# Kernel tuning notes

Measured on AMD Instinct MI355X. Metric: run time of the kernel, lower is better.

Reference implementation:

```python
import jax, jax.numpy as jnp
import numpy as np

DIM = 512
HEADS = 8
DIM_HEAD = 64
INNER = HEADS * DIM_HEAD
MAX_POS = 512


def setup_inputs() -> dict:
    key = jax.random.key(0)
    ks = jax.random.split(key, 6)
    b, n = 8, 1024
    x = jax.random.normal(ks[0], (b, n, DIM), dtype=jnp.float32)
    Wq = jax.random.normal(ks[1], (DIM, INNER), dtype=jnp.float32) * (DIM ** -0.5)
    Wkv = jax.random.normal(ks[2], (DIM, 2 * INNER), dtype=jnp.float32) * (DIM ** -0.5)
    rel_emb = jax.random.normal(ks[3], (2 * MAX_POS + 1, DIM_HEAD), dtype=jnp.float32) * 0.02
    Wo = jax.random.normal(ks[4], (INNER, DIM), dtype=jnp.float32) * (INNER ** -0.5)
    bo = jnp.zeros((DIM,), dtype=jnp.float32)
    return {"x": x, "Wq": Wq, "Wkv": Wkv, "rel_emb": rel_emb, "Wo": Wo, "bo": bo}


def reference(x, Wq, Wkv, rel_emb, Wo, bo):
    b, n, _ = x.shape
    scale = DIM_HEAD ** -0.5
    q = x @ Wq                      # [b, n, inner]
    kv = x @ Wkv                    # [b, n, 2*inner]
    k, v = jnp.split(kv, 2, axis=-1)
    # b n (h d) -> b h n d
    split_heads = lambda t: t.reshape(b, n, HEADS, DIM_HEAD).transpose(0, 2, 1, 3)
    q, k, v = split_heads(q), split_heads(k), split_heads(v)
    dots = jnp.einsum('bhid,bhjd->bhij', q, k) * scale  # [b,h,n,n]
    seq = jnp.arange(n)
    dist = jnp.clip(seq[:, None] - seq[None, :], -MAX_POS, MAX_POS) + MAX_POS  # [n,n]
    rel = rel_emb[dist]                                  # [n, n, d]
    pos_attn = jnp.einsum('bhnd,nrd->bhnr', q, rel) * scale
    dots = dots + pos_attn
    attn = jax.nn.softmax(dots, axis=-1)
    out = jnp.einsum('bhij,bhjd->bhid', attn, v)        # [b,h,n,d]
    out = out.transpose(0, 2, 1, 3).reshape(b, n, INNER)
    return out @ Wo + bo
```

## Files before the change

kernel.cpp:

```cpp
#include <hip/hip_runtime.h>

typedef __attribute__((ext_vector_type(8))) short bf16x8;
typedef __attribute__((ext_vector_type(4))) float f32x4;
typedef unsigned short u16;
typedef unsigned int u32;

#define MFMA16(a, b, c) __builtin_amdgcn_mfma_f32_16x16x32_bf16((a), (b), (c), 0, 0, 0)

__device__ __forceinline__ u16 f2b(float f) {
    u32 u = __float_as_uint(f);
    u32 r = u + 0x7fffu + ((u >> 16) & 1u);
    return (u16)(r >> 16);
}
__device__ __forceinline__ float b2f(u16 u) { return __uint_as_float(((u32)u) << 16); }

__global__ void k_f32_to_bf16(const float* __restrict__ in, u16* __restrict__ out, int n) {
    int i = (blockIdx.x * blockDim.x + threadIdx.x) * 4;
    if (i + 3 < n) {
        float4 v = *(const float4*)(in + i);
        out[i] = f2b(v.x); out[i + 1] = f2b(v.y); out[i + 2] = f2b(v.z); out[i + 3] = f2b(v.w);
    } else {
        for (int j = i; j < n; ++j) out[j] = f2b(in[j]);
    }
}

__global__ void k_make_wqkv_t(const float* __restrict__ Wq, const float* __restrict__ Wkv,
                              u16* __restrict__ wt) {
    int tid = blockIdx.x * blockDim.x + threadIdx.x;
    int k = tid & 511, n = tid >> 9;
    float v = (n < 512) ? Wq[k * 512 + n] : Wkv[k * 1024 + (n - 512)];
    wt[n * 512 + k] = f2b(v);
}

__global__ void k_make_wo_t(const float* __restrict__ Wo, u16* __restrict__ wt) {
    int tid = blockIdx.x * blockDim.x + threadIdx.x;
    int k = tid & 511, n = tid >> 9;
    wt[n * 512 + k] = f2b(Wo[k * 512 + n]);
}

__global__ __launch_bounds__(256) void k_gemm_qkv(const u16* __restrict__ A, const u16* __restrict__ Bt,
                                                  u16* __restrict__ Q, u16* __restrict__ K,
                                                  u16* __restrict__ V) {
    __shared__ u16 As[128][40];
    __shared__ u16 Bs[128][40];
    const int t = threadIdx.x, l = t & 63, w = t >> 6;
    const int wr = w >> 1, wc = w & 1, l15 = l & 15, lg = l >> 4;
    const int m0 = blockIdx.x * 128, n0 = blockIdx.y * 128;
    f32x4 acc[4][4];
#pragma unroll
    for (int i = 0; i < 4; ++i)
#pragma unroll
        for (int j = 0; j < 4; ++j) acc[i][j] = (f32x4){0.f, 0.f, 0.f, 0.f};
    const int sr = t >> 1, sko = (t & 1) * 16;
    for (int k0 = 0; k0 < 512; k0 += 32) {
        __syncthreads();
        {
            const bf16x8* pa = (const bf16x8*)(A + (size_t)(m0 + sr) * 512 + k0 + sko);
            *(bf16x8*)&As[sr][sko] = pa[0];
            *(bf16x8*)&As[sr][sko + 8] = pa[1];
            const bf16x8* pb = (const bf16x8*)(Bt + (size_t)(n0 + sr) * 512 + k0 + sko);
            *(bf16x8*)&Bs[sr][sko] = pb[0];
            *(bf16x8*)&Bs[sr][sko + 8] = pb[1];
        }
        __syncthreads();
        bf16x8 af[4], bfr[4];
#pragma unroll
        for (int rt = 0; rt < 4; ++rt) af[rt] = *(const bf16x8*)&As[wr * 64 + rt * 16 + l15][lg * 8];
#pragma unroll
        for (int ct = 0; ct < 4; ++ct) bfr[ct] = *(const bf16x8*)&Bs[wc * 64 + ct * 16 + l15][lg * 8];
#pragma unroll
        for (int rt = 0; rt < 4; ++rt)
#pragma unroll
            for (int ct = 0; ct < 4; ++ct) acc[rt][ct] = MFMA16(af[rt], bfr[ct], acc[rt][ct]);
    }
#pragma unroll
    for (int rt = 0; rt < 4; ++rt)
#pragma unroll
        for (int ct = 0; ct < 4; ++ct) {
            int n = n0 + wc * 64 + ct * 16 + l15;
            int sec = n >> 9, nn = n & 511, h = nn >> 6, d = nn & 63;
            u16* dst = (sec == 0) ? Q : ((sec == 1) ? K : V);
#pragma unroll
            for (int r = 0; r < 4; ++r) {
                int m = m0 + wr * 64 + rt * 16 + lg * 4 + r;
                int b = m >> 10, pos = m & 1023, bh = b * 8 + h;
                dst[(size_t)bh * 65536 + (size_t)pos * 64 + d] = f2b(acc[rt][ct][r]);
            }
        }
}

__global__ __launch_bounds__(256) void k_transpose_v(const u16* __restrict__ V, u16* __restrict__ Vt) {
    __shared__ u16 tile[64][72];
    const int bh = blockIdx.x >> 4, pt = blockIdx.x & 15;
    const int p0 = pt * 64;
    const int t = threadIdx.x, r = t >> 2, c0 = (t & 3) * 16;
    const bf16x8* src = (const bf16x8*)(V + (size_t)bh * 65536 + (size_t)(p0 + r) * 64 + c0);
    *(bf16x8*)&tile[r][c0] = src[0];
    *(bf16x8*)&tile[r][c0 + 8] = src[1];
    __syncthreads();
    union { u16 u[8]; bf16x8 v; } o0, o1;
#pragma unroll
    for (int ii = 0; ii < 8; ++ii) {
        o0.u[ii] = tile[c0 + ii][r];
        o1.u[ii] = tile[c0 + 8 + ii][r];
    }
    bf16x8* dst = (bf16x8*)(Vt + (size_t)bh * 65536 + (size_t)r * 1024 + p0 + c0);
    dst[0] = o0.v;
    dst[1] = o1.v;
}

__global__ __launch_bounds__(512, 4) void k_attn(const u16* __restrict__ Q, const u16* __restrict__ K,
                                                 const u16* __restrict__ Vt, const u16* __restrict__ relb,
                                                 u16* __restrict__ Ob) {
    __shared__ u16 Ks[64][72];
    __shared__ u16 Vs[64][72];
    __shared__ u16 sdw[8][16][84];
    __shared__ u16 pw[8][16][72];
    const int t = threadIdx.x, l = t & 63, w = t >> 6;
    const int l15 = l & 15, lg = l >> 4;
    const int g = (blockIdx.x & 7) * 64 + (blockIdx.x >> 3);
    const int bh = g >> 3;
    const int iw = (g & 7) * 128 + w * 16;
    const size_t hb = (size_t)bh * 65536;
    const int srow = t >> 3, scol = (t & 7) * 8;

    bf16x8 qf[2];
#pragma unroll
    for (int kf = 0; kf < 2; ++kf)
        qf[kf] = *(const bf16x8*)(Q + hb + (size_t)(iw + l15) * 64 + kf * 32 + lg * 8);

    f32x4 acc_o[4];
    float m_r[4], l_r[4];
#pragma unroll
    for (int i = 0; i < 4; ++i) {
        acc_o[i] = (f32x4){0.f, 0.f, 0.f, 0.f};
        m_r[i] = -1e30f;
        l_r[i] = 0.f;
    }

    bf16x8 kreg = *(const bf16x8*)(K + hb + (size_t)srow * 64 + scol);
    bf16x8 vreg = *(const bf16x8*)(Vt + hb + (size_t)srow * 1024 + scol);
    *(bf16x8*)&Ks[srow][scol] = kreg;
    *(bf16x8*)&Vs[srow][scol] = vreg;
    kreg = *(const bf16x8*)(K + hb + (size_t)(64 + srow) * 64 + scol);
    vreg = *(const bf16x8*)(Vt + hb + (size_t)srow * 1024 + 64 + scol);
    __syncthreads();

    for (int j0 = 0; j0 < 1024; j0 += 64) {
        f32x4 acc_s[4];
#pragma unroll
        for (int c = 0; c < 4; ++c) {
            acc_s[c] = (f32x4){0.f, 0.f, 0.f, 0.f};
#pragma unroll
            for (int kf = 0; kf < 2; ++kf) {
                bf16x8 kb = *(const bf16x8*)&Ks[c * 16 + l15][kf * 32 + lg * 8];
                acc_s[c] = MFMA16(qf[kf], kb, acc_s[c]);
            }
        }
        const int bd = iw - j0 - 63;
#pragma unroll
        for (int pt = 0; pt < 5; ++pt) {
            int tcol = pt * 16 + l15;
            int dd = bd + tcol;
            dd = dd < -512 ? -512 : (dd > 512 ? 512 : dd);
            const u16* rrow = relb + (size_t)(dd + 512) * 64;
            f32x4 a = (f32x4){0.f, 0.f, 0.f, 0.f};
#pragma unroll
            for (int kf = 0; kf < 2; ++kf) {
                bf16x8 rb = *(const bf16x8*)(rrow + kf * 32 + lg * 8);
                a = MFMA16(qf[kf], rb, a);
            }
#pragma unroll
            for (int r = 0; r < 4; ++r) sdw[w][lg * 4 + r][tcol] = f2b(a[r]);
        }
#pragma unroll
        for (int rr = 0; rr < 4; ++rr) {
            const int row = lg * 4 + rr;
            const int tb = row + 63 - l15;
            float sv[4];
#pragma unroll
            for (int c = 0; c < 4; ++c)
                sv[c] = (acc_s[c][rr] + b2f(sdw[w][row][tb - c * 16])) * 0.125f;
            float mt = fmaxf(fmaxf(sv[0], sv[1]), fmaxf(sv[2], sv[3]));
#pragma unroll
            for (int off = 1; off < 16; off <<= 1) mt = fmaxf(mt, __shfl_xor(mt, off, 64));
            float mnew = fmaxf(m_r[rr], mt);
            float alpha = __expf(m_r[rr] - mnew);
            m_r[rr] = mnew;
            float rs = 0.f;
#pragma unroll
            for (int c = 0; c < 4; ++c) {
                float pv = __expf(sv[c] - mnew);
                rs += pv;
                pw[w][row][c * 16 + l15] = f2b(pv);
            }
#pragma unroll
            for (int off = 1; off < 16; off <<= 1) rs += __shfl_xor(rs, off, 64);
            l_r[rr] = l_r[rr] * alpha + rs;
#pragma unroll
            for (int dt = 0; dt < 4; ++dt) acc_o[dt][rr] *= alpha;
        }
        bf16x8 pa[2];
#pragma unroll
        for (int kf = 0; kf < 2; ++kf) pa[kf] = *(const bf16x8*)&pw[w][l15][kf * 32 + lg * 8];
#pragma unroll
        for (int dt = 0; dt < 4; ++dt) {
#pragma unroll
            for (int kf = 0; kf < 2; ++kf) {
                bf16x8 vb = *(const bf16x8*)&Vs[dt * 16 + l15][kf * 32 + lg * 8];
                acc_o[dt] = MFMA16(pa[kf], vb, acc_o[dt]);
            }
        }
        __syncthreads();
        if (j0 + 64 < 1024) {
            *(bf16x8*)&Ks[srow][scol] = kreg;
            *(bf16x8*)&Vs[srow][scol] = vreg;
            if (j0 + 128 < 1024) {
                kreg = *(const bf16x8*)(K + hb + (size_t)(j0 + 128 + srow) * 64 + scol);
                vreg = *(const bf16x8*)(Vt + hb + (size_t)srow * 1024 + (j0 + 128) + scol);
            }
            __syncthreads();
        }
    }
    const int b = bh >> 3, h = bh & 7;
#pragma unroll
    for (int rr = 0; rr < 4; ++rr) {
        float rinv = 1.0f / l_r[rr];
        int row = lg * 4 + rr;
#pragma unroll
        for (int dt = 0; dt < 4; ++dt)
            Ob[(size_t)(b * 1024 + iw + row) * 512 + h * 64 + dt * 16 + l15] = f2b(acc_o[dt][rr] * rinv);
    }
}

__global__ __launch_bounds__(256) void k_gemm_out(const u16* __restrict__ A, const u16* __restrict__ Bt,
                                                  const float* __restrict__ bias, float* __restrict__ out) {
    __shared__ u16 As[128][40];
    __shared__ u16 Bs[128][40];
    const int t = threadIdx.x, l = t & 63, w = t >> 6;
    const int wr = w >> 1, wc = w & 1, l15 = l & 15, lg = l >> 4;
    const int m0 = blockIdx.x * 128, n0 = blockIdx.y * 128;
    f32x4 acc[4][4];
#pragma unroll
    for (int i = 0; i < 4; ++i)
#pragma unroll
        for (int j = 0; j < 4; ++j) acc[i][j] = (f32x4){0.f, 0.f, 0.f, 0.f};
    const int sr = t >> 1, sko = (t & 1) * 16;
    for (int k0 = 0; k0 < 512; k0 += 32) {
        __syncthreads();
        {
            const bf16x8* pa = (const bf16x8*)(A + (size_t)(m0 + sr) * 512 + k0 + sko);
            *(bf16x8*)&As[sr][sko] = pa[0];
            *(bf16x8*)&As[sr][sko + 8] = pa[1];
            const bf16x8* pb = (const bf16x8*)(Bt + (size_t)(n0 + sr) * 512 + k0 + sko);
            *(bf16x8*)&Bs[sr][sko] = pb[0];
            *(bf16x8*)&Bs[sr][sko + 8] = pb[1];
        }
        __syncthreads();
        bf16x8 af[4], bfr[4];
#pragma unroll
        for (int rt = 0; rt < 4; ++rt) af[rt] = *(const bf16x8*)&As[wr * 64 + rt * 16 + l15][lg * 8];
#pragma unroll
        for (int ct = 0; ct < 4; ++ct) bfr[ct] = *(const bf16x8*)&Bs[wc * 64 + ct * 16 + l15][lg * 8];
#pragma unroll
        for (int rt = 0; rt < 4; ++rt)
#pragma unroll
            for (int ct = 0; ct < 4; ++ct) acc[rt][ct] = MFMA16(af[rt], bfr[ct], acc[rt][ct]);
    }
#pragma unroll
    for (int rt = 0; rt < 4; ++rt)
#pragma unroll
        for (int ct = 0; ct < 4; ++ct) {
            int n = n0 + wc * 64 + ct * 16 + l15;
            float bv = bias[n];
#pragma unroll
            for (int r = 0; r < 4; ++r) {
                int m = m0 + wr * 64 + rt * 16 + lg * 4 + r;
                out[(size_t)m * 512 + n] = acc[rt][ct][r] + bv;
            }
        }
}

extern "C" void kernel_launch(void* const* d_in, const int* in_sizes, int n_in,
                              void* d_out, int out_size, void* d_ws, size_t ws_size,
                              hipStream_t stream) {
    const float* x    = (const float*)d_in[0];
    const float* Wq   = (const float*)d_in[1];
    const float* Wkv  = (const float*)d_in[2];
    const float* rel  = (const float*)d_in[3];
    const float* Wo   = (const float*)d_in[4];
    const float* bo   = (const float*)d_in[5];
    float* out = (float*)d_out;
    char* ws = (char*)d_ws;

    u16* xb   = (u16*)(ws + 0);
    u16* wqkv = (u16*)(ws + 8388608);
    u16* wot  = (u16*)(ws + 9961472);
    u16* relb = (u16*)(ws + 10485760);
    u16* Q    = (u16*)(ws + 10616960);
    u16* K    = (u16*)(ws + 19005568);
    u16* V    = (u16*)(ws + 27394176);
    u16* Vt   = (u16*)(ws + 35782784);
    u16* Ob   = (u16*)(ws + 44171392);

    k_f32_to_bf16<<<4096, 256, 0, stream>>>(x, xb, 4194304);
    k_f32_to_bf16<<<65, 256, 0, stream>>>(rel, relb, 65600);
    k_make_wqkv_t<<<3072, 256, 0, stream>>>(Wq, Wkv, wqkv);
    k_make_wo_t<<<1024, 256, 0, stream>>>(Wo, wot);
    k_gemm_qkv<<<dim3(64, 12), 256, 0, stream>>>(xb, wqkv, Q, K, V);
    k_transpose_v<<<1024, 256, 0, stream>>>(V, Vt);
    k_attn<<<512, 512, 0, stream>>>(Q, K, Vt, relb, Ob);
    k_gemm_out<<<dim3(64, 4), 256, 0, stream>>>(Ob, wot, bo, out);
}
```

Baseline: 145.0 us.

## Transpose attention MFMAs so softmax rows stay in registers, drop P LDS staging

Swaps the MFMA operand order so each lane holds a full query row's scores (S^T layout). Softmax then needs only two cross-lane shuffles, and P can be packed directly into registers as the B operand of the PV MFMA, with no round trip through shared memory. The relative-position band is stored as packed u32 pairs. A __syncthreads is added after the band write, occupancy hint is lowered from 4 to 2 blocks, and V is read as two 4-element halves to match the new K-index layout.

```diff
diff --git a/kernel.cpp b/kernel.cpp
--- a/kernel.cpp
+++ b/kernel.cpp
@@ -1,6 +1,7 @@
 #include <hip/hip_runtime.h>
 
 typedef __attribute__((ext_vector_type(8))) short bf16x8;
+typedef __attribute__((ext_vector_type(4))) short bf16x4;
 typedef __attribute__((ext_vector_type(4))) float f32x4;
 typedef unsigned short u16;
 typedef unsigned int u32;
@@ -13,6 +14,9 @@
     return (u16)(r >> 16);
 }
 __device__ __forceinline__ float b2f(u16 u) { return __uint_as_float(((u32)u) << 16); }
+__device__ __forceinline__ u32 packbf(float lo, float hi) {
+    return (u32)f2b(lo) | ((u32)f2b(hi) << 16);
+}
 
 __global__ void k_f32_to_bf16(const float* __restrict__ in, u16* __restrict__ out, int n) {
     int i = (blockIdx.x * blockDim.x + threadIdx.x) * 4;
@@ -109,13 +113,12 @@
     dst[1] = o1.v;
 }
 
-__global__ __launch_bounds__(512, 4) void k_attn(const u16* __restrict__ Q, const u16* __restrict__ K,
+__global__ __launch_bounds__(512, 2) void k_attn(const u16* __restrict__ Q, const u16* __restrict__ K,
                                                  const u16* __restrict__ Vt, const u16* __restrict__ relb,
                                                  u16* __restrict__ Ob) {
     __shared__ u16 Ks[64][72];
     __shared__ u16 Vs[64][72];
-    __shared__ u16 sdw[8][16][84];
-    __shared__ u16 pw[8][16][72];
+    __shared__ u32 sdw[8][16][42];
     const int t = threadIdx.x, l = t & 63, w = t >> 6;
     const int l15 = l & 15, lg = l >> 4;
     const int g = (blockIdx.x & 7) * 64 + (blockIdx.x >> 3);
@@ -130,13 +133,9 @@
         qf[kf] = *(const bf16x8*)(Q + hb + (size_t)(iw + l15) * 64 + kf * 32 + lg * 8);
 
     f32x4 acc_o[4];
-    float m_r[4], l_r[4];
-#pragma unroll
-    for (int i = 0; i < 4; ++i) {
-        acc_o[i] = (f32x4){0.f, 0.f, 0.f, 0.f};
-        m_r[i] = -1e30f;
-        l_r[i] = 0.f;
-    }
+#pragma unroll
+    for (int i = 0; i < 4; ++i) acc_o[i] = (f32x4){0.f, 0.f, 0.f, 0.f};
+    float m_r = -1e30f, l_r = 0.f;
 
     bf16x8 kreg = *(const bf16x8*)(K + hb + (size_t)srow * 64 + scol);
     bf16x8 vreg = *(const bf16x8*)(Vt + hb + (size_t)srow * 1024 + scol);
@@ -154,83 +153,98 @@
 #pragma unroll
             for (int kf = 0; kf < 2; ++kf) {
                 bf16x8 kb = *(const bf16x8*)&Ks[c * 16 + l15][kf * 32 + lg * 8];
-                acc_s[c] = MFMA16(qf[kf], kb, acc_s[c]);
+                acc_s[c] = MFMA16(kb, qf[kf], acc_s[c]);
             }
         }
         const int bd = iw - j0 - 63;
 #pragma unroll
         for (int pt = 0; pt < 5; ++pt) {
-            int tcol = pt * 16 + l15;
-            int dd = bd + tcol;
+            int dd = bd + pt * 16 + l15;
             dd = dd < -512 ? -512 : (dd > 512 ? 512 : dd);
             const u16* rrow = relb + (size_t)(dd + 512) * 64;
             f32x4 a = (f32x4){0.f, 0.f, 0.f, 0.f};
 #pragma unroll
             for (int kf = 0; kf < 2; ++kf) {
                 bf16x8 rb = *(const bf16x8*)(rrow + kf * 32 + lg * 8);
-                a = MFMA16(qf[kf], rb, a);
-            }
-#pragma unroll
-            for (int r = 0; r < 4; ++r) sdw[w][lg * 4 + r][tcol] = f2b(a[r]);
-        }
-#pragma unroll
-        for (int rr = 0; rr < 4; ++rr) {
-            const int row = lg * 4 + rr;
-            const int tb = row + 63 - l15;
-            float sv[4];
-#pragma unroll
-            for (int c = 0; c < 4; ++c)
-                sv[c] = (acc_s[c][rr] + b2f(sdw[w][row][tb - c * 16])) * 0.125f;
-            float mt = fmaxf(fmaxf(sv[0], sv[1]), fmaxf(sv[2], sv[3]));
-#pragma unroll
-            for (int off = 1; off < 16; off <<= 1) mt = fmaxf(mt, __shfl_xor(mt, off, 64));
-            float mnew = fmaxf(m_r[rr], mt);
-            float alpha = __expf(m_r[rr] - mnew);
-            m_r[rr] = mnew;
-            float rs = 0.f;
-#pragma unroll
-            for (int c = 0; c < 4; ++c) {
-                float pv = __expf(sv[c] - mnew);
-                rs += pv;
-                pw[w][row][c * 16 + l15] = f2b(pv);
-            }
-#pragma unroll
-            for (int off = 1; off < 16; off <<= 1) rs += __shfl_xor(rs, off, 64);
-            l_r[rr] = l_r[rr] * alpha + rs;
-#pragma unroll
-            for (int dt = 0; dt < 4; ++dt) acc_o[dt][rr] *= alpha;
-        }
-        bf16x8 pa[2];
-#pragma unroll
-        for (int kf = 0; kf < 2; ++kf) pa[kf] = *(const bf16x8*)&pw[w][l15][kf * 32 + lg * 8];
-#pragma unroll
-        for (int dt = 0; dt < 4; ++dt) {
+                a = MFMA16(rb, qf[kf], a);
+            }
+            int wc32 = pt * 8 + lg * 2;
+            sdw[w][l15][wc32] = packbf(a[0], a[1]);
+            sdw[w][l15][wc32 + 1] = packbf(a[2], a[3]);
+        }
+        __syncthreads();
+        float sv[4][4];
+#pragma unroll
+        for (int c = 0; c < 4; ++c)
+#pragma unroll
+            for (int r = 0; r < 4; ++r) {
+                int tt = l15 + 63 - c * 16 - lg * 4 - r;
+                u32 wv = sdw[w][l15][tt >> 1];
+                float band = b2f((u16)(wv >> ((tt & 1) * 16)));
+                sv[c][r] = (acc_s[c][r] + band) * 0.125f;
+            }
+        float mt = sv[0][0];
+#pragma unroll
+        for (int c = 0; c < 4; ++c)
+#pragma unroll
+            for (int r = 0; r < 4; ++r) mt = fmaxf(mt, sv[c][r]);
+        mt = fmaxf(mt, __shfl_xor(mt, 16, 64));
+        mt = fmaxf(mt, __shfl_xor(mt, 32, 64));
+        float mnew = fmaxf(m_r, mt);
+        float alpha = __expf(m_r - mnew);
+        m_r = mnew;
+        float p[4][4];
+        float rs = 0.f;
+#pragma unroll
+        for (int c = 0; c < 4; ++c)
+#pragma unroll
+            for (int r = 0; r < 4; ++r) {
+                p[c][r] = __expf(sv[c][r] - mnew);
+                rs += p[c][r];
+            }
+        rs += __shfl_xor(rs, 16, 64);
+        rs += __shfl_xor(rs, 32, 64);
+        l_r = l_r * alpha + rs;
+#pragma unroll
+        for (int dt = 0; dt < 4; ++dt)
+#pragma unroll
+            for (int r = 0; r < 4; ++r) acc_o[dt][r] *= alpha;
+        union { u32 wd[4]; bf16x8 v; } pb[2];
+#pragma unroll
+        for (int kf = 0; kf < 2; ++kf)
+#pragma unroll
+            for (int h = 0; h < 4; ++h) {
+                int c = kf * 2 + (h >> 1), r0 = (h & 1) * 2;
+                pb[kf].wd[h] = packbf(p[c][r0], p[c][r0 + 1]);
+            }
+#pragma unroll
+        for (int dt = 0; dt < 4; ++dt)
 #pragma unroll
             for (int kf = 0; kf < 2; ++kf) {
-                bf16x8 vb = *(const bf16x8*)&Vs[dt * 16 + l15][kf * 32 + lg * 8];
-                acc_o[dt] = MFMA16(pa[kf], vb, acc_o[dt]);
-            }
-        }
+                union { bf16x4 h[2]; bf16x8 v; } vb;
+                vb.h[0] = *(const bf16x4*)&Vs[dt * 16 + l15][kf * 32 + lg * 4];
+                vb.h[1] = *(const bf16x4*)&Vs[dt * 16 + l15][kf * 32 + 16 + lg * 4];
+                acc_o[dt] = MFMA16(vb.v, pb[kf].v, acc_o[dt]);
+            }
         __syncthreads();
         if (j0 + 64 < 1024) {
             *(bf16x8*)&Ks[srow][scol] = kreg;
             *(bf16x8*)&Vs[srow][scol] = vreg;
-            if (j0 + 128 < 1024) {
-                kreg = *(const bf16x8*)(K + hb + (size_t)(j0 + 128 + srow) * 64 + scol);
-                vreg = *(const bf16x8*)(Vt + hb + (size_t)srow * 1024 + (j0 + 128) + scol);
-            }
+            int jp = j0 / 64 + 2;
+            if (jp > 15) jp = 15;
+            kreg = *(const bf16x8*)(K + hb + (size_t)(jp * 64 + srow) * 64 + scol);
+            vreg = *(const bf16x8*)(Vt + hb + (size_t)srow * 1024 + jp * 64 + scol);
             __syncthreads();
         }
     }
     const int b = bh >> 3, h = bh & 7;
-#pragma unroll
-    for (int rr = 0; rr < 4; ++rr) {
-        float rinv = 1.0f / l_r[rr];
-        int row = lg * 4 + rr;
-#pragma unroll
-        for (int dt = 0; dt < 4; ++dt)
-            Ob[(size_t)(b * 1024 + iw + row) * 512 + h * 64 + dt * 16 + l15] = f2b(acc_o[dt][rr] * rinv);
-    }
+    const float rinv = 1.0f / l_r;
+    const size_t rowbase = (size_t)(b * 1024 + iw + l15) * 512 + h * 64;
+#pragma unroll
+    for (int dt = 0; dt < 4; ++dt)
+#pragma unroll
+        for (int r = 0; r < 4; ++r)
+            Ob[rowbase + dt * 16 + lg * 4 + r] = f2b(acc_o[dt][r] * rinv);
 }
 
 __global__ __launch_bounds__(256) void k_gemm_out(const u16* __restrict__ A, const u16* __restrict__ Bt,
```

Measured after the change: 159.1 us. 1.1x slower.
